# Kernel optimization log

Hardware: AMD Instinct MI355X
Metric: run time of the kernel (lower is better)

The kernel has to match this reference:

```python
import jax, jax.numpy as jnp
import numpy as np

B, N, H, EMB, BOT = 32, 128, 64, 64, 64


def _node2edge(x):
    # x: (B, N, F) -> edges (B, N*N, 2F); edge e=i*N+j holds [x[j] (receiver), x[i] (sender)]
    b, n, f = x.shape
    recv = jnp.broadcast_to(x[:, None, :, :], (b, n, n, f))  # varies with j
    send = jnp.broadcast_to(x[:, :, None, :], (b, n, n, f))  # varies with i
    return jnp.concatenate([recv, send], axis=-1).reshape(b, n * n, 2 * f)


def _edge2node(e, n):
    # e: (B, N*N, F); receiver of edge i*N+j is j -> sum over i; divide by FEATURE dim (faithful to source)
    b, _, f = e.shape
    return e.reshape(b, n, n, f).sum(axis=1) / f


def _lin(x, w, b):
    return x @ w + b


def setup_inputs() -> dict:
    key = jax.random.key(0)
    ks = jax.random.split(key, 24)

    def w(k, i, o):
        return jax.random.normal(k, (i, o), jnp.float32) / np.sqrt(i)

    def bias(k, o):
        return jax.random.normal(k, (o,), jnp.float32) * 0.01

    return {
        "h_states": jax.random.normal(ks[0], (B, N, H), jnp.float32),
        "end_pos": jax.random.normal(ks[1], (B, N, 2), jnp.float32),
        "se_w": w(ks[2], 2, EMB), "se_b": bias(ks[3], EMB),
        "s1_w": w(ks[4], 2 * H + EMB, 128), "s1_b": bias(ks[5], 128),
        "s2_w": w(ks[6], 128, H), "s2_b": bias(ks[7], H),
        "n1_w": w(ks[8], H, 128), "n1_b": bias(ks[9], 128),
        "n2_w": w(ks[10], 128, H), "n2_b": bias(ks[11], H),
        "e1_w": w(ks[12], 2 * H, 128), "e1_b": bias(ks[13], 128),
        "e2_w": w(ks[14], 128, H), "e2_b": bias(ks[15], H),
        "f1_w": w(ks[16], H, 128), "f1_b": bias(ks[17], 128),
        "f2_w": w(ks[18], 128, BOT), "f2_b": bias(ks[19], BOT),
    }


def reference(h_states, end_pos, se_w, se_b, s1_w, s1_b, s2_w, s2_b,
              n1_w, n1_b, n2_w, n2_b, e1_w, e1_b, e2_w, e2_b,
              f1_w, f1_b, f2_w, f2_b):
    b, n, _ = h_states.shape
    # relative positions: pos[i] - pos[j] for edge i*N+j -> (B, N*N, 2)
    rel_pos = (end_pos[:, :, None, :] - end_pos[:, None, :, :]).reshape(b, n * n, 2)
    rel_emb = _lin(rel_pos, se_w, se_b)  # (B, N*N, EMB)

    edge_feat = jnp.concatenate([_node2edge(h_states), rel_emb], axis=-1)  # (B, N*N, 2H+EMB)
    # nmp_mlp_start: two linears, no activation (activation=None), dropout inert in eval
    edge_feat = _lin(_lin(edge_feat, s1_w, s1_b), s2_w, s2_b)  # (B, N*N, H)

    # nmp_layers=2 -> one (node mlp, edge mlp) pair, no activations
    node_feat = _lin(_lin(_edge2node(edge_feat, n), n1_w, n1_b), n2_w, n2_b)
    edge_feat = _lin(_lin(_node2edge(node_feat), e1_w, e1_b), e2_w, e2_b)

    # nmp_mlp_end: Linear -> ReLU -> Linear -> ReLU
    x = _edge2node(edge_feat, n)
    x = jax.nn.relu(_lin(x, f1_w, f1_b))
    x = jax.nn.relu(_lin(x, f2_w, f2_b))
    return x  # (B, N, BOT)
```

## Files before the change

kernel.cpp:

```cpp
#include <hip/hip_runtime.h>

enum : int {
  WS_H1 = 0,
  WS_H2 = 8192,
  WS_H3 = 8448,
  WS_END = 12544
};

__global__ __launch_bounds__(256) void k_prep(
    const float* __restrict__ h, const float* __restrict__ pos,
    const float* __restrict__ se_w, const float* __restrict__ se_b,
    const float* __restrict__ s1_w, const float* __restrict__ s1_b,
    const float* __restrict__ s2_w, const float* __restrict__ s2_b,
    const float* __restrict__ n1_w, const float* __restrict__ n1_b,
    const float* __restrict__ n2_w, const float* __restrict__ n2_b,
    const float* __restrict__ e1_w, const float* __restrict__ e1_b,
    const float* __restrict__ e2_w, const float* __restrict__ e2_b,
    const float* __restrict__ f1_w, const float* __restrict__ f1_b,
    float* __restrict__ ws)
{
  __shared__ __align__(16) float smem[1280];
  int blk = blockIdx.x, t = threadIdx.x;

  if (blk < 32) {
    float* VA = smem;
    float* VB = smem + 640;
    const int c0 = blk * 4;
    const int j = t & 3, rb = t >> 2;
    if (t < 256) { int k = t >> 2, jj = t & 3;
      VA[k * 5 + jj] = f1_w[k * 128 + c0 + jj];
    }
    __syncthreads();
    { float a0 = 0.f, a1 = 0.f;
      #pragma unroll 16
      for (int k = 0; k < 64; ++k) {
        float v = VA[k*5 + j];
        a0 = fmaf(e2_w[rb*64 + k],      v, a0);
        a1 = fmaf(e2_w[(rb+64)*64 + k], v, a1);
      }
      VB[rb*5+j] = a0; VB[(rb+64)*5+j] = a1; }
    __syncthreads();
    { float a = 0.f;
      #pragma unroll 16
      for (int k = 0; k < 128; ++k) a = fmaf(e1_w[rb*128 + k], VB[k*5 + j], a);
      VA[rb*5+j] = a; }
    __syncthreads();
    { float a0 = 0.f, a1 = 0.f;
      #pragma unroll 16
      for (int k = 0; k < 64; ++k) {
        float v = VA[k*5 + j];
        a0 = fmaf(n2_w[rb*64 + k],      v, a0);
        a1 = fmaf(n2_w[(rb+64)*64 + k], v, a1);
      }
      VB[rb*5+j] = a0; VB[(rb+64)*5+j] = a1; }
    __syncthreads();
    { float a = 0.f;
      #pragma unroll 16
      for (int k = 0; k < 128; ++k) a = fmaf(n1_w[rb*128 + k], VB[k*5 + j], a);
      VA[rb*5+j] = a; }
    __syncthreads();
    { float a0 = 0.f, a1 = 0.f;
      #pragma unroll 16
      for (int k = 0; k < 64; ++k) {
        float v = VA[k*5 + j];
        a0 = fmaf(s2_w[rb*64 + k],      v, a0);
        a1 = fmaf(s2_w[(rb+64)*64 + k], v, a1);
      }
      VB[rb*5+j] = a0; VB[(rb+64)*5+j] = a1; }
    __syncthreads();
    { float a = 0.f, z = 0.f;
      #pragma unroll 16
      for (int k = 0; k < 128; ++k) {
        float v = VB[k*5 + j];
        a = fmaf(s1_w[rb*128 + k],       v, a);
        z = fmaf(s1_w[(128+rb)*128 + k], v, z);
      }
      ws[WS_H1 + rb*128 + c0 + j] = 4.f * a;
      VA[rb*5+j] = z; }
    __syncthreads();
    if (t < 8) {
      int r2 = t >> 2, jj = t & 3;
      float a = 0.f;
      #pragma unroll 16
      for (int k = 0; k < 64; ++k) a = fmaf(se_w[r2*64 + k], VA[k*5 + jj], a);
      ws[WS_H2 + r2*128 + c0 + jj] = -4.f * a;
    }
  } else {
    int b = blk - 32;
    float* part = smem;
    float* sX = smem + 256;
    float* sP = smem + 320;
    float* L0 = smem + 384;
    float* L1 = smem + 512;
    float* L2 = smem + 640;
    float* L3 = smem + 768;
    float* M0 = smem + 896;
    float* M1 = smem + 960;
    { int k = t & 63, g = t >> 6; float s = 0.f;
      #pragma unroll 8
      for (int jn = g * 32; jn < g * 32 + 32; ++jn) s += h[(b * 128 + jn) * 64 + k];
      part[t] = s; }
    __syncthreads();
    if (t < 64) sX[t] = (part[t] + part[64 + t]) + (part[128 + t] + part[192 + t]);
    else if (t < 128) {
      int l = t - 64;
      const float* pb = pos + b * 256;
      float s = (pb[l] + pb[64 + l]) + (pb[128 + l] + pb[192 + l]);
      #pragma unroll
      for (int m = 2; m <= 32; m <<= 1) s += __shfl_xor(s, m, 64);
      if (l < 2) sP[l] = s;
    }
    __syncthreads();
    { int g = t >> 7, o = t & 127;
      if (g == 0) {
        float a = 0.f, kk = 0.f;
        #pragma unroll
        for (int k = 0; k < 64; ++k) {
          a  = fmaf(sX[k],   s1_w[k * 128 + o],         a);
          kk = fmaf(se_b[k], s1_w[(128 + k) * 128 + o], kk);
        }
        L0[o] = a; L1[o] = kk + s1_b[o];
      } else {
        float p0 = sP[0], p1 = sP[1];
        float a = 0.f, yy = 0.f;
        #pragma unroll
        for (int k = 0; k < 64; ++k) {
          a = fmaf(sX[k], s1_w[(64 + k) * 128 + o], a);
          float qk = fmaf(p1, se_w[64 + k], p0 * se_w[k]);
          yy = fmaf(qk, s1_w[(128 + k) * 128 + o], yy);
        }
        L2[o] = a; L3[o] = yy;
      } }
    __syncthreads();
    if (t < 128) { int g = t >> 6, c = t & 63;
      float a = 0.f;
      if (g == 0) {
        #pragma unroll
        for (int o = 0; o < 128; ++o) {
          float r2 = fmaf(2.f, L1[o], (L2[o] + L3[o]) * (1.f / 64.f));
          a = fmaf(r2, s2_w[o * 64 + c], a);
        }
        M0[c] = a + 2.f * s2_b[c];
      } else {
        #pragma unroll
        for (int o = 0; o < 128; ++o)
          a = fmaf(2.f * (L0[o] - L3[o]), s2_w[o * 64 + c], a);
        M1[c] = a;
      } }
    __syncthreads();
    { int g = t >> 7, o = t & 127;
      float a = 0.f;
      if (g == 0) {
        #pragma unroll
        for (int k = 0; k < 64; ++k) a = fmaf(M0[k], n1_w[k * 128 + o], a);
        L0[o] = a + n1_b[o];
      } else {
        #pragma unroll
        for (int k = 0; k < 64; ++k) a = fmaf(M1[k], n1_w[k * 128 + o], a);
        L1[o] = a;
      } }
    __syncthreads();
    if (t < 128) { int g = t >> 6, c = t & 63;
      float a = 0.f;
      if (g == 0) {
        #pragma unroll
        for (int o = 0; o < 128; ++o) a = fmaf(L0[o], n2_w[o * 64 + c], a);
        M0[c] = a + n2_b[c];
      } else {
        #pragma unroll
        for (int o = 0; o < 128; ++o) a = fmaf(L1[o], n2_w[o * 64 + c], a);
        M1[c] = a;
      } }
    __syncthreads();
    { int g = t >> 7, o = t & 127;
      float a = 0.f;
      if (g == 0) {
        #pragma unroll
        for (int k = 0; k < 64; ++k) a = fmaf(M0[k], e1_w[k * 128 + o], a);
        L0[o] = a;
      } else {
        #pragma unroll
        for (int k = 0; k < 64; ++k) {
          float nb = fmaf(128.f, M0[k], M1[k]);
          a = fmaf(nb, e1_w[(64 + k) * 128 + o], a);
        }
        L1[o] = a;
      } }
    __syncthreads();
    if (t < 64) { float a = 0.f;
      #pragma unroll
      for (int o = 0; o < 128; ++o) {
        float gv = fmaf(L1[o], (1.f / 64.f), fmaf(2.f, L0[o], 2.f * e1_b[o]));
        a = fmaf(gv, e2_w[o * 64 + t], a);
      }
      M0[t] = a + 2.f * e2_b[t]; }
    __syncthreads();
    if (t < 128) { float a = 0.f;
      #pragma unroll
      for (int k = 0; k < 64; ++k) a = fmaf(M0[k], f1_w[k * 128 + t], a);
      ws[WS_H3 + b * 128 + t] = a + f1_b[t]; }
  }
}

__global__ __launch_bounds__(256) void k_main(
    const float* __restrict__ h, const float* __restrict__ pos,
    const float* __restrict__ f2_w, const float* __restrict__ f2_b,
    const float* __restrict__ ws, float* __restrict__ out)
{
  __shared__ __align__(16) float lH1[64 * 128];
  __shared__ __align__(16) float lx[16 * 64];
  __shared__ float lp[16 * 2];
  __shared__ __align__(16) float lh1[16 * 128];
  int blk = blockIdx.x, t = threadIdx.x;
  int b = blk >> 3, j0 = (blk & 7) * 16;
  for (int i = t; i < 2048; i += 256) ((float4*)lH1)[i] = ((const float4*)(ws + WS_H1))[i];
  ((float4*)lx)[t] = ((const float4*)(h + (size_t)(b * 128 + j0) * 64))[t];
  if (t < 32) lp[t] = pos[(b * 128 + j0) * 2 + t];
  __syncthreads();
  {
    int d = t & 127, g = t >> 7, n0 = g * 8;
    float h3v = ws[WS_H3 + b * 128 + d];
    float h2a = ws[WS_H2 + d], h2b = ws[WS_H2 + 128 + d];
    float acc[8];
    #pragma unroll
    for (int i = 0; i < 8; ++i)
      acc[i] = h3v + lp[(n0 + i) * 2] * h2a + lp[(n0 + i) * 2 + 1] * h2b;
    #pragma unroll 4
    for (int k = 0; k < 64; k += 4) {
      float h0 = lH1[k * 128 + d], h1v = lH1[(k + 1) * 128 + d],
            h2v = lH1[(k + 2) * 128 + d], h3w = lH1[(k + 3) * 128 + d];
      #pragma unroll
      for (int i = 0; i < 8; ++i) {
        float4 xv = *(const float4*)&lx[(n0 + i) * 64 + k];
        acc[i] = fmaf(xv.x, h0, fmaf(xv.y, h1v, fmaf(xv.z, h2v, fmaf(xv.w, h3w, acc[i]))));
      }
    }
    #pragma unroll
    for (int i = 0; i < 8; ++i) lh1[(n0 + i) * 128 + d] = fmaxf(acc[i], 0.f);
  }
  __syncthreads();
  {
    int d = t & 63, g = t >> 6, n0 = g * 4;
    float acc[4];
    float bias = f2_b[d];
    #pragma unroll
    for (int i = 0; i < 4; ++i) acc[i] = bias;
    #pragma unroll 4
    for (int k = 0; k < 128; k += 4) {
      float f0 = f2_w[k * 64 + d], f1v = f2_w[(k + 1) * 64 + d],
            f2v = f2_w[(k + 2) * 64 + d], f3v = f2_w[(k + 3) * 64 + d];
      #pragma unroll
      for (int i = 0; i < 4; ++i) {
        float4 hv = *(const float4*)&lh1[(n0 + i) * 128 + k];
        acc[i] = fmaf(hv.x, f0, fmaf(hv.y, f1v, fmaf(hv.z, f2v, fmaf(hv.w, f3v, acc[i]))));
      }
    }
    #pragma unroll
    for (int i = 0; i < 4; ++i)
      out[(size_t)(b * 128 + j0 + n0 + i) * 64 + d] = fmaxf(acc[i], 0.f);
  }
}

extern "C" void kernel_launch(void* const* d_in, const int* in_sizes, int n_in,
                              void* d_out, int out_size, void* d_ws, size_t ws_size,
                              hipStream_t stream) {
  const float* h    = (const float*)d_in[0];
  const float* pos  = (const float*)d_in[1];
  const float* se_w = (const float*)d_in[2];
  const float* se_b = (const float*)d_in[3];
  const float* s1_w = (const float*)d_in[4];
  const float* s1_b = (const float*)d_in[5];
  const float* s2_w = (const float*)d_in[6];
  const float* s2_b = (const float*)d_in[7];
  const float* n1_w = (const float*)d_in[8];
  const float* n1_b = (const float*)d_in[9];
  const float* n2_w = (const float*)d_in[10];
  const float* n2_b = (const float*)d_in[11];
  const float* e1_w = (const float*)d_in[12];
  const float* e1_b = (const float*)d_in[13];
  const float* e2_w = (const float*)d_in[14];
  const float* e2_b = (const float*)d_in[15];
  const float* f1_w = (const float*)d_in[16];
  const float* f1_b = (const float*)d_in[17];
  const float* f2_w = (const float*)d_in[18];
  const float* f2_b = (const float*)d_in[19];
  float* ws = (float*)d_ws;
  float* out = (float*)d_out;

  hipLaunchKernelGGL(k_prep, dim3(64), dim3(256), 0, stream,
                     h, pos, se_w, se_b, s1_w, s1_b, s2_w, s2_b,
                     n1_w, n1_b, n2_w, n2_b, e1_w, e1_b, e2_w, e2_b,
                     f1_w, f1_b, ws);
  hipLaunchKernelGGL(k_main, dim3(256), dim3(256), 0, stream, h, pos, f2_w, f2_b, ws, out);
}
```

Before: 27.43 us.

## Stage weight matrices in shared memory and split prep work across more blocks

Measured after the change: 29.71 us. +8.3%, slower.

```diff
diff --git a/kernel.cpp b/kernel.cpp
--- a/kernel.cpp
+++ b/kernel.cpp
@@ -19,74 +19,95 @@
     const float* __restrict__ f1_w, const float* __restrict__ f1_b,
     float* __restrict__ ws)
 {
-  __shared__ __align__(16) float smem[1280];
+  __shared__ __align__(16) float smem[9472];
   int blk = blockIdx.x, t = threadIdx.x;
 
-  if (blk < 32) {
-    float* VA = smem;
-    float* VB = smem + 640;
-    const int c0 = blk * 4;
-    const int j = t & 3, rb = t >> 2;
-    if (t < 256) { int k = t >> 2, jj = t & 3;
-      VA[k * 5 + jj] = f1_w[k * 128 + c0 + jj];
+  if (blk < 64) {
+    float* W  = smem;
+    float* VA = smem + 8320;
+    float* VB = smem + 8704;
+    float* PT = smem + 9088;
+    const int c0 = blk * 2;
+    const int j = t & 1, rb = t >> 1;
+
+    #define STAGE_W_128x64(ptr) \
+      { _Pragma("unroll") for (int it = 0; it < 8; ++it) { \
+          int i = t + it * 256; int row = i >> 4, col = (i & 15) * 4; \
+          *(float4*)&W[row * 65 + col] = *(const float4*)((ptr) + row * 64 + col); } }
+    #define STAGE_W_64x128(ptr) \
+      { _Pragma("unroll") for (int it = 0; it < 8; ++it) { \
+          int i = t + it * 256; int row = i >> 5, col = (i & 31) * 4; \
+          *(float4*)&W[row * 129 + col] = *(const float4*)((ptr) + row * 128 + col); } }
+    #define MUL_128x64(IN, OUT) \
+      { float a0=0.f,a1=0.f,a2=0.f,a3=0.f; \
+        _Pragma("unroll") for (int k = 0; k < 16; ++k) { \
+          a0 = fmaf(W[rb*65 + k],      IN[(k)*3 + j],      a0); \
+          a1 = fmaf(W[rb*65 + 16 + k], IN[(16 + k)*3 + j], a1); \
+          a2 = fmaf(W[rb*65 + 32 + k], IN[(32 + k)*3 + j], a2); \
+          a3 = fmaf(W[rb*65 + 48 + k], IN[(48 + k)*3 + j], a3); } \
+        OUT[rb*3 + j] = (a0 + a1) + (a2 + a3); }
+    #define MUL_64x128_PART(IN) \
+      { float a0=0.f,a1=0.f,a2=0.f,a3=0.f; int r = rb & 63, kb = (rb >> 6) * 64; \
+        _Pragma("unroll") for (int k = 0; k < 16; ++k) { \
+          a0 = fmaf(W[r*129 + kb + k],      IN[(kb + k)*3 + j],      a0); \
+          a1 = fmaf(W[r*129 + kb + 16 + k], IN[(kb + 16 + k)*3 + j], a1); \
+          a2 = fmaf(W[r*129 + kb + 32 + k], IN[(kb + 32 + k)*3 + j], a2); \
+          a3 = fmaf(W[r*129 + kb + 48 + k], IN[(kb + 48 + k)*3 + j], a3); } \
+        PT[rb*3 + j] = (a0 + a1) + (a2 + a3); }
+
+    if (t < 128) { int k = t >> 1; VA[k * 3 + (t & 1)] = f1_w[k * 128 + c0 + (t & 1)]; }
+    STAGE_W_128x64(e2_w);
+    __syncthreads();
+    MUL_128x64(VA, VB);
+    __syncthreads();
+    STAGE_W_64x128(e1_w);
+    __syncthreads();
+    MUL_64x128_PART(VB);
+    __syncthreads();
+    if (rb < 64) VA[rb * 3 + j] = PT[rb * 3 + j] + PT[(rb + 64) * 3 + j];
+    STAGE_W_128x64(n2_w);
+    __syncthreads();
+    MUL_128x64(VA, VB);
+    __syncthreads();
+    STAGE_W_64x128(n1_w);
+    __syncthreads();
+    MUL_64x128_PART(VB);
+    __syncthreads();
+    if (rb < 64) VA[rb * 3 + j] = PT[rb * 3 + j] + PT[(rb + 64) * 3 + j];
+    STAGE_W_128x64(s2_w);
+    __syncthreads();
+    MUL_128x64(VA, VB);
+    __syncthreads();
+    STAGE_W_64x128(s1_w);
+    __syncthreads();
+    MUL_64x128_PART(VB);
+    __syncthreads();
+    if (rb < 64)
+      ws[WS_H1 + rb * 128 + c0 + j] = 4.f * (PT[rb * 3 + j] + PT[(rb + 64) * 3 + j]);
+    STAGE_W_64x128(s1_w + 128 * 128);
+    __syncthreads();
+    MUL_64x128_PART(VB);
+    __syncthreads();
+    if (rb < 64) VA[rb * 3 + j] = PT[rb * 3 + j] + PT[(rb + 64) * 3 + j];
+    __syncthreads();
+    if (t < 4) {
+      int r2 = t >> 1, jj = t & 1;
+      float a0 = 0.f, a1 = 0.f, a2 = 0.f, a3 = 0.f;
+      #pragma unroll
+      for (int k = 0; k < 16; ++k) {
+        a0 = fmaf(se_w[r2 * 64 + k],      VA[(k) * 3 + jj],      a0);
+        a1 = fmaf(se_w[r2 * 64 + 16 + k], VA[(16 + k) * 3 + jj], a1);
+        a2 = fmaf(se_w[r2 * 64 + 32 + k], VA[(32 + k) * 3 + jj], a2);
+        a3 = fmaf(se_w[r2 * 64 + 48 + k], VA[(48 + k) * 3 + jj], a3);
+      }
+      ws[WS_H2 + r2 * 128 + c0 + jj] = -4.f * ((a0 + a1) + (a2 + a3));
     }
-    __syncthreads();
-    { float a0 = 0.f, a1 = 0.f;
-      #pragma unroll 16
-      for (int k = 0; k < 64; ++k) {
-        float v = VA[k*5 + j];
-        a0 = fmaf(e2_w[rb*64 + k],      v, a0);
-        a1 = fmaf(e2_w[(rb+64)*64 + k], v, a1);
-      }
-      VB[rb*5+j] = a0; VB[(rb+64)*5+j] = a1; }
-    __syncthreads();
-    { float a = 0.f;
-      #pragma unroll 16
-      for (int k = 0; k < 128; ++k) a = fmaf(e1_w[rb*128 + k], VB[k*5 + j], a);
-      VA[rb*5+j] = a; }
-    __syncthreads();
-    { float a0 = 0.f, a1 = 0.f;
-      #pragma unroll 16
-      for (int k = 0; k < 64; ++k) {
-        float v = VA[k*5 + j];
-        a0 = fmaf(n2_w[rb*64 + k],      v, a0);
-        a1 = fmaf(n2_w[(rb+64)*64 + k], v, a1);
-      }
-      VB[rb*5+j] = a0; VB[(rb+64)*5+j] = a1; }
-    __syncthreads();
-    { float a = 0.f;
-      #pragma unroll 16
-      for (int k = 0; k < 128; ++k) a = fmaf(n1_w[rb*128 + k], VB[k*5 + j], a);
-      VA[rb*5+j] = a; }
-    __syncthreads();
-    { float a0 = 0.f, a1 = 0.f;
-      #pragma unroll 16
-      for (int k = 0; k < 64; ++k) {
-        float v = VA[k*5 + j];
-        a0 = fmaf(s2_w[rb*64 + k],      v, a0);
-        a1 = fmaf(s2_w[(rb+64)*64 + k], v, a1);
-      }
-      VB[rb*5+j] = a0; VB[(rb+64)*5+j] = a1; }
-    __syncthreads();
-    { float a = 0.f, z = 0.f;
-      #pragma unroll 16
-      for (int k = 0; k < 128; ++k) {
-        float v = VB[k*5 + j];
-        a = fmaf(s1_w[rb*128 + k],       v, a);
-        z = fmaf(s1_w[(128+rb)*128 + k], v, z);
-      }
-      ws[WS_H1 + rb*128 + c0 + j] = 4.f * a;
-      VA[rb*5+j] = z; }
-    __syncthreads();
-    if (t < 8) {
-      int r2 = t >> 2, jj = t & 3;
-      float a = 0.f;
-      #pragma unroll 16
-      for (int k = 0; k < 64; ++k) a = fmaf(se_w[r2*64 + k], VA[k*5 + jj], a);
-      ws[WS_H2 + r2*128 + c0 + jj] = -4.f * a;
-    }
+    #undef STAGE_W_128x64
+    #undef STAGE_W_64x128
+    #undef MUL_128x64
+    #undef MUL_64x128_PART
   } else {
-    int b = blk - 32;
+    int b = blk - 64;
     float* part = smem;
     float* sX = smem + 256;
     float* sP = smem + 320;
@@ -113,92 +134,107 @@
     __syncthreads();
     { int g = t >> 7, o = t & 127;
       if (g == 0) {
-        float a = 0.f, kk = 0.f;
-        #pragma unroll
-        for (int k = 0; k < 64; ++k) {
-          a  = fmaf(sX[k],   s1_w[k * 128 + o],         a);
-          kk = fmaf(se_b[k], s1_w[(128 + k) * 128 + o], kk);
-        }
-        L0[o] = a; L1[o] = kk + s1_b[o];
+        float a0 = 0.f, a1 = 0.f, k0 = 0.f, k1 = 0.f;
+        #pragma unroll
+        for (int k = 0; k < 32; ++k) {
+          a0 = fmaf(sX[k],        s1_w[k * 128 + o],                a0);
+          a1 = fmaf(sX[32 + k],   s1_w[(32 + k) * 128 + o],         a1);
+          k0 = fmaf(se_b[k],      s1_w[(128 + k) * 128 + o],        k0);
+          k1 = fmaf(se_b[32 + k], s1_w[(160 + k) * 128 + o],        k1);
+        }
+        L0[o] = a0 + a1; L1[o] = (k0 + k1) + s1_b[o];
       } else {
         float p0 = sP[0], p1 = sP[1];
-        float a = 0.f, yy = 0.f;
-        #pragma unroll
-        for (int k = 0; k < 64; ++k) {
-          a = fmaf(sX[k], s1_w[(64 + k) * 128 + o], a);
-          float qk = fmaf(p1, se_w[64 + k], p0 * se_w[k]);
-          yy = fmaf(qk, s1_w[(128 + k) * 128 + o], yy);
-        }
-        L2[o] = a; L3[o] = yy;
+        float a0 = 0.f, a1 = 0.f, y0 = 0.f, y1 = 0.f;
+        #pragma unroll
+        for (int k = 0; k < 32; ++k) {
+          a0 = fmaf(sX[k],      s1_w[(64 + k) * 128 + o], a0);
+          a1 = fmaf(sX[32 + k], s1_w[(96 + k) * 128 + o], a1);
+          float qa = fmaf(p1, se_w[64 + k], p0 * se_w[k]);
+          float qb = fmaf(p1, se_w[96 + k], p0 * se_w[32 + k]);
+          y0 = fmaf(qa, s1_w[(128 + k) * 128 + o], y0);
+          y1 = fmaf(qb, s1_w[(160 + k) * 128 + o], y1);
+        }
+        L2[o] = a0 + a1; L3[o] = y0 + y1;
       } }
     __syncthreads();
     if (t < 128) { int g = t >> 6, c = t & 63;
-      float a = 0.f;
+      float a0 = 0.f, a1 = 0.f;
       if (g == 0) {
         #pragma unroll
-        for (int o = 0; o < 128; ++o) {
-          float r2 = fmaf(2.f, L1[o], (L2[o] + L3[o]) * (1.f / 64.f));
-          a = fmaf(r2, s2_w[o * 64 + c], a);
-        }
-        M0[c] = a + 2.f * s2_b[c];
+        for (int o = 0; o < 64; ++o) {
+          float ra = fmaf(2.f, L1[o],      (L2[o] + L3[o]) * (1.f / 64.f));
+          float rb2 = fmaf(2.f, L1[64 + o], (L2[64 + o] + L3[64 + o]) * (1.f / 64.f));
+          a0 = fmaf(ra,  s2_w[o * 64 + c],        a0);
+          a1 = fmaf(rb2, s2_w[(64 + o) * 64 + c], a1);
+        }
+        M0[c] = (a0 + a1) + 2.f * s2_b[c];
       } else {
         #pragma unroll
-        for (int o = 0; o < 128; ++o)
-          a = fmaf(2.f * (L0[o] - L3[o]), s2_w[o * 64 + c], a);
-        M1[c] = a;
+        for (int o = 0; o < 64; ++o) {
+          a0 = fmaf(2.f * (L0[o] - L3[o]),           s2_w[o * 64 + c],        a0);
+          a1 = fmaf(2.f * (L0[64 + o] - L3[64 + o]), s2_w[(64 + o) * 64 + c], a1);
+        }
+        M1[c] = a0 + a1;
       } }
     __syncthreads();
     { int g = t >> 7, o = t & 127;
-      float a = 0.f;
+      float a0 = 0.f, a1 = 0.f;
+      const float* mv = (g == 0) ? M0 : M1;
+      #pragma unroll
+      for (int k = 0; k < 32; ++k) {
+        a0 = fmaf(mv[k],      n1_w[k * 128 + o],        a0);
+        a1 = fmaf(mv[32 + k], n1_w[(32 + k) * 128 + o], a1);
+      }
+      if (g == 0) L0[o] = (a0 + a1) + n1_b[o]; else L1[o] = a0 + a1; }
+    __syncthreads();
+    if (t < 128) { int g = t >> 6, c = t & 63;
+      const float* lv = (g == 0) ? L0 : L1;
+      float a0 = 0.f, a1 = 0.f;
+      #pragma unroll
+      for (int o = 0; o < 64; ++o) {
+        a0 = fmaf(lv[o],      n2_w[o * 64 + c],        a0);
+        a1 = fmaf(lv[64 + o], n2_w[(64 + o) * 64 + c], a1);
+      }
+      if (g == 0) M0[c] = (a0 + a1) + n2_b[c]; else M1[c] = a0 + a1; }
+    __syncthreads();
+    { int g = t >> 7, o = t & 127;
+      float a0 = 0.f, a1 = 0.f;
       if (g == 0) {
         #pragma unroll
-        for (int k = 0; k < 64; ++k) a = fmaf(M0[k], n1_w[k * 128 + o], a);
-        L0[o] = a + n1_b[o];
+        for (int k = 0; k < 32; ++k) {
+          a0 = fmaf(M0[k],      e1_w[k * 128 + o],        a0);
+          a1 = fmaf(M0[32 + k], e1_w[(32 + k) * 128 + o], a1);
+        }
+        L0[o] = a0 + a1;
       } else {
         #pragma unroll
-        for (int k = 0; k < 64; ++k) a = fmaf(M1[k], n1_w[k * 128 + o], a);
-        L1[o] = a;
+        for (int k = 0; k < 32; ++k) {
+          float na = fmaf(128.f, M0[k],      M1[k]);
+          float nb = fmaf(128.f, M0[32 + k], M1[32 + k]);
+          a0 = fmaf(na, e1_w[(64 + k) * 128 + o], a0);
+          a1 = fmaf(nb, e1_w[(96 + k) * 128 + o], a1);
+        }
+        L1[o] = a0 + a1;
       } }
     __syncthreads();
-    if (t < 128) { int g = t >> 6, c = t & 63;
-      float a = 0.f;
-      if (g == 0) {
-        #pragma unroll
-        for (int o = 0; o < 128; ++o) a = fmaf(L0[o], n2_w[o * 64 + c], a);
-        M0[c] = a + n2_b[c];
-      } else {
-        #pragma unroll
-        for (int o = 0; o < 128; ++o) a = fmaf(L1[o], n2_w[o * 64 + c], a);
-        M1[c] = a;
-      } }
-    __syncthreads();
-    { int g = t >> 7, o = t & 127;
-      float a = 0.f;
-      if (g == 0) {
-        #pragma unroll
-        for (int k = 0; k < 64; ++k) a = fmaf(M0[k], e1_w[k * 128 + o], a);
-        L0[o] = a;
-      } else {
-        #pragma unroll
-        for (int k = 0; k < 64; ++k) {
-          float nb = fmaf(128.f, M0[k], M1[k]);
-          a = fmaf(nb, e1_w[(64 + k) * 128 + o], a);
-        }
-        L1[o] = a;
-      } }
-    __syncthreads();
-    if (t < 64) { float a = 0.f;
-      #pragma unroll
-      for (int o = 0; o < 128; ++o) {
-        float gv = fmaf(L1[o], (1.f / 64.f), fmaf(2.f, L0[o], 2.f * e1_b[o]));
-        a = fmaf(gv, e2_w[o * 64 + t], a);
-      }
-      M0[t] = a + 2.f * e2_b[t]; }
-    __syncthreads();
-    if (t < 128) { float a = 0.f;
-      #pragma unroll
-      for (int k = 0; k < 64; ++k) a = fmaf(M0[k], f1_w[k * 128 + t], a);
-      ws[WS_H3 + b * 128 + t] = a + f1_b[t]; }
+    if (t < 64) { float a0 = 0.f, a1 = 0.f;
+      #pragma unroll
+      for (int o = 0; o < 64; ++o) {
+        float ga = fmaf(L1[o],      (1.f / 64.f), fmaf(2.f, L0[o],      2.f * e1_b[o]));
+        float gb = fmaf(L1[64 + o], (1.f / 64.f), fmaf(2.f, L0[64 + o], 2.f * e1_b[64 + o]));
+        a0 = fmaf(ga, e2_w[o * 64 + t],        a0);
+        a1 = fmaf(gb, e2_w[(64 + o) * 64 + t], a1);
+      }
+      M0[t] = (a0 + a1) + 2.f * e2_b[t]; }
+    __syncthreads();
+    if (t < 128) { float a0 = 0.f, a1 = 0.f;
+      #pragma unroll
+      for (int k = 0; k < 32; ++k) {
+        a0 = fmaf(M0[k],      f1_w[k * 128 + t],        a0);
+        a1 = fmaf(M0[32 + k], f1_w[(32 + k) * 128 + t], a1);
+      }
+      ws[WS_H3 + b * 128 + t] = (a0 + a1) + f1_b[t]; }
   }
 }
 
@@ -287,7 +323,7 @@
   float* ws = (float*)d_ws;
   float* out = (float*)d_out;
 
-  hipLaunchKernelGGL(k_prep, dim3(64), dim3(256), 0, stream,
+  hipLaunchKernelGGL(k_prep, dim3(96), dim3(256), 0, stream,
                      h, pos, se_w, se_b, s1_w, s1_b, s2_w, s2_b,
                      n1_w, n1_b, n2_w, n2_b, e1_w, e1_b, e2_w, e2_b,
                      f1_w, f1_b, ws);
```
